# Kernel tuning notes

Measured on AMD Instinct MI355X. Metric: run time of the kernel, lower is better.

## Reference

```python
import jax, jax.numpy as jnp
import numpy as np

NUM_C = 1000
B, L = 8, 1024
D, H, NB, DFF = 512, 8, 4, 2048
DK = D // H
EPS = 1e-5


def _ln(x, s, b):
    mu = jnp.mean(x, axis=-1, keepdims=True)
    var = jnp.mean((x - mu) ** 2, axis=-1, keepdims=True)
    return (x - mu) * jax.lax.rsqrt(var + EPS) * s + b


def setup_inputs() -> dict:
    key = jax.random.key(0)
    ks = iter(jax.random.split(key, 64))

    def nrm(shape, scale=0.02):
        return jax.random.normal(next(ks), shape, dtype=jnp.float32) * scale

    inp = {
        "q": jax.random.randint(next(ks), (B, L), 0, NUM_C),
        "r": jax.random.randint(next(ks), (B, L), 0, 2),
        # embeddings
        "ctx_emb": nrm((NUM_C * 2, D)),
        "val_emb": nrm((NUM_C * 2, D)),
        "skill_emb": nrm((NUM_C, D)),
        "pos_emb": nrm((L, D)),
        # attention projections, stacked over blocks
        "Wq": nrm((NB, D, D)), "bq": jnp.zeros((NB, D)),
        "Wk": nrm((NB, D, D)), "bk": jnp.zeros((NB, D)),
        "Wv": nrm((NB, D, D)), "bv": jnp.zeros((NB, D)),
        "Wo": nrm((NB, D, D)), "bo": jnp.zeros((NB, D)),
        # layer norms (ctx / val streams, pre- and post-FFN)
        "ln1c_s": jnp.ones((NB, D)), "ln1c_b": jnp.zeros((NB, D)),
        "ln1v_s": jnp.ones((NB, D)), "ln1v_b": jnp.zeros((NB, D)),
        "ln2c_s": jnp.ones((NB, D)), "ln2c_b": jnp.zeros((NB, D)),
        "ln2v_s": jnp.ones((NB, D)), "ln2v_b": jnp.zeros((NB, D)),
        # FFNs
        "fc1c_W": nrm((NB, D, DFF)), "fc1c_b": jnp.zeros((NB, DFF)),
        "fc2c_W": nrm((NB, DFF, D)), "fc2c_b": jnp.zeros((NB, D)),
        "fc1v_W": nrm((NB, D, DFF)), "fc1v_b": jnp.zeros((NB, DFF)),
        "fc2v_W": nrm((NB, DFF, D)), "fc2v_b": jnp.zeros((NB, D)),
        # prediction head: [3D -> DFF -> 256 -> 1]
        "hW1": nrm((3 * D, DFF)), "hb1": jnp.zeros((DFF,)),
        "hW2": nrm((DFF, 256)), "hb2": jnp.zeros((256,)),
        "hW3": nrm((256, 1)), "hb3": jnp.zeros((1,)),
    }
    return inp


def reference(q, r, ctx_emb, val_emb, skill_emb, pos_emb,
              Wq, bq, Wk, bk, Wv, bv, Wo, bo,
              ln1c_s, ln1c_b, ln1v_s, ln1v_b,
              ln2c_s, ln2c_b, ln2v_s, ln2v_b,
              fc1c_W, fc1c_b, fc2c_W, fc2c_b,
              fc1v_W, fc1v_b, fc2v_W, fc2v_b,
              hW1, hb1, hW2, hb2, hW3, hb3):
    inter = q + NUM_C * r                       # [B, L] interaction ids
    pos = pos_emb[None, :L, :]
    ctx = ctx_emb[inter] + pos                  # [B, L, D]
    val = val_emb[inter] + pos                  # [B, L, D]
    causal = jnp.tril(jnp.ones((L, L), dtype=bool))
    scale = 1.0 / (DK ** 0.5)

    for i in range(NB):
        # dual-stream MHA: Q,K from ctx; V from val
        Q = (ctx @ Wq[i] + bq[i]).reshape(B, L, H, DK)
        K = (ctx @ Wk[i] + bk[i]).reshape(B, L, H, DK)
        V = (val @ Wv[i] + bv[i]).reshape(B, L, H, DK)
        # fp32 scores (as in torch source), mask==0 -> -inf, softmax
        scores = jnp.einsum('bqhd,bkhd->bhqk', Q.astype(jnp.float32),
                            K.astype(jnp.float32)) * scale
        scores = jnp.where(causal, scores, -jnp.inf)
        attn = jax.nn.softmax(scores, axis=-1)  # dropout = identity (eval)
        out = jnp.einsum('bhqk,bkhd->bqhd', attn, V).reshape(B, L, D)
        out = out @ Wo[i] + bo[i]
        # shared attn output added to both streams, separate norms
        ctx = _ln(ctx + out, ln1c_s[i], ln1c_b[i])
        val = _ln(val + out, ln1v_s[i], ln1v_b[i])
        # dual FFNs
        f_ctx = jax.nn.relu(ctx @ fc1c_W[i] + fc1c_b[i]) @ fc2c_W[i] + fc2c_b[i]
        ctx = _ln(ctx + f_ctx, ln2c_s[i], ln2c_b[i])
        f_val = jax.nn.relu(val @ fc1v_W[i] + fc1v_b[i]) @ fc2v_W[i] + fc2v_b[i]
        val = _ln(val + f_val, ln2v_s[i], ln2v_b[i])

    feat = jnp.concatenate([ctx, val, skill_emb[q]], axis=-1)  # [B, L, 3D]
    h = jax.nn.relu(feat @ hW1 + hb1)
    h = jax.nn.relu(h @ hW2 + hb2)
    logits = (h @ hW3 + hb3)[..., 0]
    return jax.nn.sigmoid(logits)               # [B, L] p(correct)
```

## Files before the change

### kernel.cpp

```cpp
#include <hip/hip_runtime.h>
#include <hip/hip_bf16.h>
#include <math.h>

#define TOK 8192
#define DM 512
#define NH 8
#define DKH 64
#define DFFN 2048
#define SEQ 1024
#define NBLK 4
#define NUMC 1000

typedef __attribute__((ext_vector_type(8))) short bf16x8;
typedef __attribute__((ext_vector_type(4))) float f32x4;
typedef __hip_bfloat16 bf16;

__device__ __forceinline__ void gload_lds16(const ushort* g, ushort* l) {
    __builtin_amdgcn_global_load_lds(
        (const __attribute__((address_space(1))) void*)g,
        (__attribute__((address_space(3))) void*)l, 16, 0, 0);
}

__global__ __launch_bounds__(256) void embed_kernel(
    const int* __restrict__ q, const int* __restrict__ r,
    const float* __restrict__ ctx_emb, const float* __restrict__ val_emb,
    const float* __restrict__ pos_emb,
    float* __restrict__ ctx32, float* __restrict__ val32,
    bf16* __restrict__ ctx16, bf16* __restrict__ val16)
{
    const int t = blockIdx.x;
    const int inter = q[t] + NUMC * r[t];
    const int l = t & (SEQ - 1);
    const float* ce = ctx_emb + (size_t)inter * DM;
    const float* ve = val_emb + (size_t)inter * DM;
    const float* pe = pos_emb + (size_t)l * DM;
    const size_t o = (size_t)t * DM;
    for (int d = threadIdx.x; d < DM; d += 256) {
        float p = pe[d];
        float c = ce[d] + p;
        float v = ve[d] + p;
        ctx32[o + d] = c; val32[o + d] = v;
        ctx16[o + d] = __float2bfloat16(c);
        val16[o + d] = __float2bfloat16(v);
    }
}

__global__ __launch_bounds__(256) void transpose_kernel(
    const float* __restrict__ src, bf16* __restrict__ dst,
    int K, int N, long sb, long db)
{
    __shared__ float t[32][33];
    src += (long)blockIdx.z * sb;
    dst += (long)blockIdx.z * db;
    const int n0 = blockIdx.x * 32;
    const int k0 = blockIdx.y * 32;
    const int tx = threadIdx.x;
    const int ty = threadIdx.y;
    for (int i = ty; i < 32; i += 8) t[i][tx] = src[(size_t)(k0 + i) * N + n0 + tx];
    __syncthreads();
    for (int i = ty; i < 32; i += 8)
        dst[(size_t)(n0 + i) * K + k0 + tx] = __float2bfloat16(t[tx][i]);
}

__global__ __launch_bounds__(256) void vtrans_kernel(
    const bf16* __restrict__ in, bf16* __restrict__ outp)
{
    __shared__ ushort T[64 * 66];
    const int ktile = blockIdx.x;
    const int bh = blockIdx.y;
    const int b = bh >> 3, h = bh & 7;
    const int t = threadIdx.x;
    const int key = t >> 2, c0 = (t & 3) * 16;
    const bf16* src = in + (size_t)(b * SEQ + ktile * 64 + key) * 512 + h * 64 + c0;
    *(bf16x8*)&T[key * 66 + c0] = *(const bf16x8*)src;
    *(bf16x8*)&T[key * 66 + c0 + 8] = *(const bf16x8*)(src + 8);
    __syncthreads();
    const int d = t >> 2, k0 = (t & 3) * 16;
    bf16x8 w0, w1;
#pragma unroll
    for (int j = 0; j < 8; ++j) w0[j] = ((short*)T)[(k0 + j) * 66 + d];
#pragma unroll
    for (int j = 0; j < 8; ++j) w1[j] = ((short*)T)[(k0 + 8 + j) * 66 + d];
    bf16* dst = outp + (size_t)(bh * 64 + d) * SEQ + ktile * 64 + k0;
    *(bf16x8*)dst = w0;
    *(bf16x8*)(dst + 8) = w1;
}

template<int BN, bool OUTBF16>
__global__ __launch_bounds__(256, 2) void mfma_gemm(
    const ushort* __restrict__ A, const ushort* __restrict__ Bt,
    const float* __restrict__ bias1, const float* __restrict__ bias2, int split,
    void* __restrict__ Cv, int N, int K, int relu,
    const ushort* __restrict__ A1, const ushort* __restrict__ Bt1,
    const float* __restrict__ bias1_1, void* __restrict__ Cv1)
{
    if (blockIdx.z) { A = A1; Bt = Bt1; bias1 = bias1_1; Cv = Cv1; }
    constexpr int MI = (BN == 128) ? 4 : 2;
    __shared__ ushort As[128 * 32];
    __shared__ ushort Bs[BN * 32];
    const int tid = threadIdx.x;
    const int wave = tid >> 6;
    const int lane = tid & 63;
    const int ln = lane & 15;
    const int kq = lane >> 4;
    const int nx = gridDim.x;
    const int lin = blockIdx.x + nx * blockIdx.y;
    const int loc = lin >> 3;
    const int mdiv = loc / nx;
    const int bm = ((lin & 7) + 8 * mdiv) * 128;
    const int bn = (loc - mdiv * nx) * BN;
    const int wr = (BN == 128) ? (wave >> 1) * 64 : wave * 32;
    const int wc = (BN == 128) ? (wave & 1) * 64 : 0;

    const int srow = tid >> 2;
    const int scol = (tid & 3) * 8;
    const ushort* Ag0 = A + (size_t)(bm + srow) * K + scol;
    const ushort* Ag1 = A + (size_t)(bm + 64 + srow) * K + scol;
    const ushort* Bg0 = Bt + (size_t)(bn + srow) * K + scol;
    const ushort* Bg1 = (BN == 128) ? (Bt + (size_t)(bn + 64 + srow) * K + scol) : nullptr;
    ushort* AsW0 = As + wave * 512;
    ushort* AsW1 = As + 2048 + wave * 512;
    ushort* BsW0 = Bs + wave * 512;
    ushort* BsW1 = Bs + 2048 + wave * 512;

    f32x4 acc[MI][4];
#pragma unroll
    for (int i = 0; i < MI; ++i)
#pragma unroll
        for (int j = 0; j < 4; ++j) acc[i][j] = (f32x4){0.f, 0.f, 0.f, 0.f};

    for (int k0 = 0; k0 < K; k0 += 32) {
        __syncthreads();
        gload_lds16(Ag0 + k0, AsW0);
        gload_lds16(Ag1 + k0, AsW1);
        gload_lds16(Bg0 + k0, BsW0);
        if (BN == 128) gload_lds16(Bg1 + k0, BsW1);
        __syncthreads();
        bf16x8 bfr[4];
#pragma unroll
        for (int j = 0; j < 4; ++j)
            bfr[j] = *(const bf16x8*)&Bs[(wc + j * 16 + ln) * 32 + kq * 8];
#pragma unroll
        for (int i = 0; i < MI; ++i) {
            const bf16x8 af = *(const bf16x8*)&As[(wr + i * 16 + ln) * 32 + kq * 8];
#pragma unroll
            for (int j = 0; j < 4; ++j)
                acc[i][j] = __builtin_amdgcn_mfma_f32_16x16x32_bf16(af, bfr[j], acc[i][j], 0, 0, 0);
        }
    }

#pragma unroll
    for (int i = 0; i < MI; ++i) {
        const int rowb = bm + wr + i * 16 + kq * 4;
#pragma unroll
        for (int j = 0; j < 4; ++j) {
            const int colg = bn + wc + j * 16 + ln;
            const float bv = (colg < split) ? bias1[colg] : bias2[colg - split];
#pragma unroll
            for (int rr = 0; rr < 4; ++rr) {
                float v = acc[i][j][rr] + bv;
                if (relu) v = fmaxf(v, 0.f);
                if (OUTBF16)
                    ((bf16*)Cv)[(size_t)(rowb + rr) * N + colg] = __float2bfloat16(v);
                else
                    ((float*)Cv)[(size_t)(rowb + rr) * N + colg] = v;
            }
        }
    }
}

__global__ __launch_bounds__(256) void attn_kernel(
    const bf16* __restrict__ QK, const bf16* __restrict__ Vt,
    bf16* __restrict__ Og)
{
    __shared__ ushort Qs[64 * 68];
    __shared__ ushort Ks[64 * 68];
    __shared__ ushort Vs[64 * 68];
    __shared__ ushort Ps[4 * 16 * 68];

    const int tid = threadIdx.x;
    const int wave = tid >> 6, lane = tid & 63;
    const int ln = lane & 15, kq = lane >> 4;
    const int lin = blockIdx.x + 16 * blockIdx.y;
    const int loc = lin >> 3;
    const int qt = loc & 15;
    const int bh = (lin & 7) + 8 * (loc >> 4);
    const int b = bh >> 3, h = bh & 7;

    const int srow = tid >> 2;
    const int sc0 = (tid & 3) * 16;
    {
        const bf16* src = QK + (size_t)(b * SEQ + qt * 64 + srow) * 1024 + h * 64 + sc0;
        *(bf16x8*)&Qs[srow * 68 + sc0] = *(const bf16x8*)src;
        *(bf16x8*)&Qs[srow * 68 + sc0 + 8] = *(const bf16x8*)(src + 8);
    }

    float m2[4], lsum[4];
    f32x4 oacc[4];
#pragma unroll
    for (int r = 0; r < 4; ++r) { m2[r] = -INFINITY; lsum[r] = 0.f; oacc[r] = (f32x4){0.f,0.f,0.f,0.f}; }
    const float sc2 = 0.125f * 1.4426950408889634f;

    for (int kt = 0; kt <= qt; ++kt) {
        __syncthreads();
        {
            const bf16* ksrc = QK + (size_t)(b * SEQ + kt * 64 + srow) * 1024 + 512 + h * 64 + sc0;
            *(bf16x8*)&Ks[srow * 68 + sc0] = *(const bf16x8*)ksrc;
            *(bf16x8*)&Ks[srow * 68 + sc0 + 8] = *(const bf16x8*)(ksrc + 8);
            const bf16* vsrc = Vt + (size_t)(bh * 64 + srow) * SEQ + kt * 64 + sc0;
            *(bf16x8*)&Vs[srow * 68 + sc0] = *(const bf16x8*)vsrc;
            *(bf16x8*)&Vs[srow * 68 + sc0 + 8] = *(const bf16x8*)(vsrc + 8);
        }
        __syncthreads();

        const bf16x8 aq0 = *(const bf16x8*)&Qs[(wave * 16 + ln) * 68 + kq * 8];
        const bf16x8 aq1 = *(const bf16x8*)&Qs[(wave * 16 + ln) * 68 + 32 + kq * 8];
        f32x4 s[4];
#pragma unroll
        for (int c = 0; c < 4; ++c) {
            const bf16x8 bk0 = *(const bf16x8*)&Ks[(c * 16 + ln) * 68 + kq * 8];
            const bf16x8 bk1 = *(const bf16x8*)&Ks[(c * 16 + ln) * 68 + 32 + kq * 8];
            s[c] = (f32x4){0.f, 0.f, 0.f, 0.f};
            s[c] = __builtin_amdgcn_mfma_f32_16x16x32_bf16(aq0, bk0, s[c], 0, 0, 0);
            s[c] = __builtin_amdgcn_mfma_f32_16x16x32_bf16(aq1, bk1, s[c], 0, 0, 0);
        }
        if (kt == qt) {
#pragma unroll
            for (int c = 0; c < 4; ++c)
#pragma unroll
                for (int r = 0; r < 4; ++r) {
                    const int qg = wave * 16 + kq * 4 + r;
                    const int jg = c * 16 + ln;
                    s[c][r] = (jg <= qg) ? s[c][r] * sc2 : -INFINITY;
                }
        } else {
#pragma unroll
            for (int c = 0; c < 4; ++c)
#pragma unroll
                for (int r = 0; r < 4; ++r) s[c][r] *= sc2;
        }
        float alpha[4];
#pragma unroll
        for (int r = 0; r < 4; ++r) {
            float v = fmaxf(fmaxf(s[0][r], s[1][r]), fmaxf(s[2][r], s[3][r]));
            v = fmaxf(v, __shfl_xor(v, 1));
            v = fmaxf(v, __shfl_xor(v, 2));
            v = fmaxf(v, __shfl_xor(v, 4));
            v = fmaxf(v, __shfl_xor(v, 8));
            const float mn = fmaxf(m2[r], v);
            alpha[r] = exp2f(m2[r] - mn);
            m2[r] = mn;
        }
        float rs[4] = {0.f, 0.f, 0.f, 0.f};
#pragma unroll
        for (int c = 0; c < 4; ++c)
#pragma unroll
            for (int r = 0; r < 4; ++r) {
                const float pv = exp2f(s[c][r] - m2[r]);
                rs[r] += pv;
                *(bf16*)&Ps[wave * 1088 + (kq * 4 + r) * 68 + c * 16 + ln] = __float2bfloat16(pv);
            }
#pragma unroll
        for (int r = 0; r < 4; ++r) {
            float v = rs[r];
            v += __shfl_xor(v, 1);
            v += __shfl_xor(v, 2);
            v += __shfl_xor(v, 4);
            v += __shfl_xor(v, 8);
            lsum[r] = lsum[r] * alpha[r] + v;
        }
#pragma unroll
        for (int c2 = 0; c2 < 4; ++c2)
#pragma unroll
            for (int r = 0; r < 4; ++r) oacc[c2][r] *= alpha[r];
        const bf16x8 ap0 = *(const bf16x8*)&Ps[wave * 1088 + ln * 68 + kq * 8];
        const bf16x8 ap1 = *(const bf16x8*)&Ps[wave * 1088 + ln * 68 + 32 + kq * 8];
#pragma unroll
        for (int c2 = 0; c2 < 4; ++c2) {
            const bf16x8 bv0 = *(const bf16x8*)&Vs[(c2 * 16 + ln) * 68 + kq * 8];
            const bf16x8 bv1 = *(const bf16x8*)&Vs[(c2 * 16 + ln) * 68 + 32 + kq * 8];
            oacc[c2] = __builtin_amdgcn_mfma_f32_16x16x32_bf16(ap0, bv0, oacc[c2], 0, 0, 0);
            oacc[c2] = __builtin_amdgcn_mfma_f32_16x16x32_bf16(ap1, bv1, oacc[c2], 0, 0, 0);
        }
    }
    float inv[4];
#pragma unroll
    for (int r = 0; r < 4; ++r) inv[r] = 1.f / lsum[r];
#pragma unroll
    for (int c2 = 0; c2 < 4; ++c2)
#pragma unroll
        for (int r = 0; r < 4; ++r)
            Og[(size_t)(b * SEQ + qt * 64 + wave * 16 + kq * 4 + r) * 512 + h * 64 + c2 * 16 + ln]
                = __float2bfloat16(oacc[c2][r] * inv[r]);
}

__global__ __launch_bounds__(256) void lnp_kernel(
    const float* __restrict__ x0, const bf16* __restrict__ r0, const float* __restrict__ s0,
    const float* __restrict__ b0, float* __restrict__ of0, bf16* __restrict__ oh0,
    const float* __restrict__ x1, const bf16* __restrict__ r1, const float* __restrict__ s1,
    const float* __restrict__ b1, float* __restrict__ of1, bf16* __restrict__ oh1)
{
    const float* x = x0; const bf16* res = r0; const float* s = s0; const float* bb = b0;
    float* of = of0; bf16* oh = oh0;
    if (blockIdx.y) { x = x1; res = r1; s = s1; bb = b1; of = of1; oh = oh1; }
    __shared__ float w1[4], w2[4];
    const size_t o = (size_t)blockIdx.x * DM;
    const int i0 = threadIdx.x, i1 = threadIdx.x + 256;
    const float v0 = x[o + i0] + __bfloat162float(res[o + i0]);
    const float v1 = x[o + i1] + __bfloat162float(res[o + i1]);
    float sum = v0 + v1;
#pragma unroll
    for (int off = 32; off; off >>= 1) sum += __shfl_down(sum, off);
    if ((threadIdx.x & 63) == 0) w1[threadIdx.x >> 6] = sum;
    __syncthreads();
    const float mu = (w1[0] + w1[1] + w1[2] + w1[3]) * (1.f / DM);
    const float d0 = v0 - mu, d1 = v1 - mu;
    float vs = d0 * d0 + d1 * d1;
#pragma unroll
    for (int off = 32; off; off >>= 1) vs += __shfl_down(vs, off);
    if ((threadIdx.x & 63) == 0) w2[threadIdx.x >> 6] = vs;
    __syncthreads();
    const float rstd = rsqrtf((w2[0] + w2[1] + w2[2] + w2[3]) * (1.f / DM) + 1e-5f);
    const float o0 = d0 * rstd * s[i0] + bb[i0];
    const float o1 = d1 * rstd * s[i1] + bb[i1];
    of[o + i0] = o0; of[o + i1] = o1;
    oh[o + i0] = __float2bfloat16(o0);
    oh[o + i1] = __float2bfloat16(o1);
}

__global__ __launch_bounds__(256) void gather_kernel(
    const bf16* __restrict__ ctx16, const bf16* __restrict__ val16,
    const float* __restrict__ skill, const int* __restrict__ q,
    bf16* __restrict__ feat)
{
    const int t = blockIdx.x;
    const float* sp = skill + (size_t)q[t] * DM;
    const bf16* cp = ctx16 + (size_t)t * DM;
    const bf16* vp = val16 + (size_t)t * DM;
    bf16* fp = feat + (size_t)t * (3 * DM);
    for (int d = threadIdx.x; d < DM; d += 256) {
        fp[d] = cp[d];
        fp[DM + d] = vp[d];
        fp[2 * DM + d] = __float2bfloat16(sp[d]);
    }
}

__global__ __launch_bounds__(256) void logits_kernel(
    const float* __restrict__ h2, const float* __restrict__ w,
    const float* __restrict__ bptr, float* __restrict__ out)
{
    __shared__ float w1[4];
    const int t = blockIdx.x;
    float sum = h2[(size_t)t * 256 + threadIdx.x] * w[threadIdx.x];
#pragma unroll
    for (int off = 32; off; off >>= 1) sum += __shfl_down(sum, off);
    if ((threadIdx.x & 63) == 0) w1[threadIdx.x >> 6] = sum;
    __syncthreads();
    if (threadIdx.x == 0) {
        const float logit = w1[0] + w1[1] + w1[2] + w1[3] + bptr[0];
        out[t] = 1.f / (1.f + __expf(-logit));
    }
}

extern "C" void kernel_launch(void* const* d_in, const int* in_sizes, int n_in,
                              void* d_out, int out_size, void* d_ws, size_t ws_size,
                              hipStream_t stream)
{
    const int*   q         = (const int*)d_in[0];
    const int*   r         = (const int*)d_in[1];
    const float* ctx_emb   = (const float*)d_in[2];
    const float* val_emb   = (const float*)d_in[3];
    const float* skill_emb = (const float*)d_in[4];
    const float* pos_emb   = (const float*)d_in[5];
    const float* Wq = (const float*)d_in[6];
    const float* bq = (const float*)d_in[7];
    const float* Wk = (const float*)d_in[8];
    const float* bk = (const float*)d_in[9];
    const float* Wv = (const float*)d_in[10];
    const float* bv = (const float*)d_in[11];
    const float* Wo = (const float*)d_in[12];
    const float* bo = (const float*)d_in[13];
    const float* ln1c_s = (const float*)d_in[14];
    const float* ln1c_b = (const float*)d_in[15];
    const float* ln1v_s = (const float*)d_in[16];
    const float* ln1v_b = (const float*)d_in[17];
    const float* ln2c_s = (const float*)d_in[18];
    const float* ln2c_b = (const float*)d_in[19];
    const float* ln2v_s = (const float*)d_in[20];
    const float* ln2v_b = (const float*)d_in[21];
    const float* fc1c_W = (const float*)d_in[22];
    const float* fc1c_b = (const float*)d_in[23];
    const float* fc2c_W = (const float*)d_in[24];
    const float* fc2c_b = (const float*)d_in[25];
    const float* fc1v_W = (const float*)d_in[26];
    const float* fc1v_b = (const float*)d_in[27];
    const float* fc2v_W = (const float*)d_in[28];
    const float* fc2v_b = (const float*)d_in[29];
    const float* hW1 = (const float*)d_in[30];
    const float* hb1 = (const float*)d_in[31];
    const float* hW2 = (const float*)d_in[32];
    const float* hb2 = (const float*)d_in[33];
    const float* hW3 = (const float*)d_in[34];
    const float* hb3 = (const float*)d_in[35];
    float* out = (float*)d_out;

    char* p = (char*)d_ws;
    auto alloc = [&](size_t bytes) { char* ret = p; p += bytes; return ret; };
    float* ctx32 = (float*)alloc(16777216);
    float* val32 = (float*)alloc(16777216);
    bf16*  ob16c = (bf16*)alloc(8388608);
    bf16*  ob16v = (bf16*)alloc(8388608);
    bf16*  ctx16 = (bf16*)alloc(8388608);
    bf16*  val16 = (bf16*)alloc(8388608);
    bf16*  qk16  = (bf16*)alloc(16777216);
    bf16*  v16   = (bf16*)alloc(8388608);
    bf16*  vt16  = (bf16*)alloc(8388608);
    bf16*  att16 = (bf16*)alloc(8388608);
    bf16*  mid16c = (bf16*)alloc(33554432);
    bf16*  qkT   = (bf16*)alloc(4194304);
    bf16*  vT    = (bf16*)alloc(2097152);
    bf16*  oT    = (bf16*)alloc(2097152);
    bf16*  fc1cT = (bf16*)alloc(8388608);
    bf16*  fc2cT = (bf16*)alloc(8388608);
    bf16*  fc1vT = (bf16*)alloc(8388608);
    bf16*  fc2vT = (bf16*)alloc(8388608);
    bf16*  hW1T  = (bf16*)alloc(6291456);
    bf16*  hW2T  = (bf16*)alloc(1048576);
    bf16*  mid16v = qk16;
    bf16*  feat16 = qk16;
    float* h2     = (float*)vt16;

    const dim3 tb(32, 8);
    transpose_kernel<<<dim3(16, 16, 4), tb, 0, stream>>>(Wq, qkT,          512, 512, 262144, 524288);
    transpose_kernel<<<dim3(16, 16, 4), tb, 0, stream>>>(Wk, qkT + 262144, 512, 512, 262144, 524288);
    transpose_kernel<<<dim3(16, 16, 4), tb, 0, stream>>>(Wv, vT, 512, 512, 262144, 262144);
    transpose_kernel<<<dim3(16, 16, 4), tb, 0, stream>>>(Wo, oT, 512, 512, 262144, 262144);
    transpose_kernel<<<dim3(64, 16, 4), tb, 0, stream>>>(fc1c_W, fc1cT, 512, 2048, 1048576, 1048576);
    transpose_kernel<<<dim3(16, 64, 4), tb, 0, stream>>>(fc2c_W, fc2cT, 2048, 512, 1048576, 1048576);
    transpose_kernel<<<dim3(64, 16, 4), tb, 0, stream>>>(fc1v_W, fc1vT, 512, 2048, 1048576, 1048576);
    transpose_kernel<<<dim3(16, 64, 4), tb, 0, stream>>>(fc2v_W, fc2vT, 2048, 512, 1048576, 1048576);
    transpose_kernel<<<dim3(64, 48, 1), tb, 0, stream>>>(hW1, hW1T, 1536, 2048, 0, 0);
    transpose_kernel<<<dim3(8, 64, 1),  tb, 0, stream>>>(hW2, hW2T, 2048, 256, 0, 0);

    embed_kernel<<<TOK, 256, 0, stream>>>(q, r, ctx_emb, val_emb, pos_emb,
                                          ctx32, val32, ctx16, val16);

    for (int i = 0; i < NBLK; ++i) {
        mfma_gemm<128, true><<<dim3(8, 64), 256, 0, stream>>>(
            (const ushort*)ctx16, (const ushort*)(qkT + (size_t)i * 524288),
            bq + i * DM, bk + i * DM, 512, qk16, 1024, 512, 0,
            nullptr, nullptr, nullptr, nullptr);
        mfma_gemm<64, true><<<dim3(8, 64), 256, 0, stream>>>(
            (const ushort*)val16, (const ushort*)(vT + (size_t)i * 262144),
            bv + i * DM, nullptr, 1 << 30, v16, 512, 512, 0,
            nullptr, nullptr, nullptr, nullptr);
        vtrans_kernel<<<dim3(16, 64), 256, 0, stream>>>(v16, vt16);
        attn_kernel<<<dim3(16, 64), 256, 0, stream>>>(qk16, vt16, att16);
        mfma_gemm<64, true><<<dim3(8, 64), 256, 0, stream>>>(
            (const ushort*)att16, (const ushort*)(oT + (size_t)i * 262144),
            bo + i * DM, nullptr, 1 << 30, ob16c, 512, 512, 0,
            nullptr, nullptr, nullptr, nullptr);
        lnp_kernel<<<dim3(TOK, 2), 256, 0, stream>>>(
            ctx32, ob16c, ln1c_s + i * DM, ln1c_b + i * DM, ctx32, ctx16,
            val32, ob16c, ln1v_s + i * DM, ln1v_b + i * DM, val32, val16);
        mfma_gemm<128, true><<<dim3(16, 64, 2), 256, 0, stream>>>(
            (const ushort*)ctx16, (const ushort*)(fc1cT + (size_t)i * 1048576),
            fc1c_b + i * DFFN, nullptr, 1 << 30, mid16c, 2048, 512, 1,
            (const ushort*)val16, (const ushort*)(fc1vT + (size_t)i * 1048576),
            fc1v_b + i * DFFN, mid16v);
        mfma_gemm<128, true><<<dim3(4, 64, 2), 256, 0, stream>>>(
            (const ushort*)mid16c, (const ushort*)(fc2cT + (size_t)i * 1048576),
            fc2c_b + i * DM, nullptr, 1 << 30, ob16c, 512, 2048, 0,
            (const ushort*)mid16v, (const ushort*)(fc2vT + (size_t)i * 1048576),
            fc2v_b + i * DM, ob16v);
        lnp_kernel<<<dim3(TOK, 2), 256, 0, stream>>>(
            ctx32, ob16c, ln2c_s + i * DM, ln2c_b + i * DM, ctx32, ctx16,
            val32, ob16v, ln2v_s + i * DM, ln2v_b + i * DM, val32, val16);
    }

    gather_kernel<<<TOK, 256, 0, stream>>>(ctx16, val16, skill_emb, q, feat16);
    mfma_gemm<128, true><<<dim3(16, 64), 256, 0, stream>>>(
        (const ushort*)feat16, (const ushort*)hW1T, hb1, nullptr, 1 << 30, mid16c, 2048, 1536, 1,
        nullptr, nullptr, nullptr, nullptr);
    mfma_gemm<64, false><<<dim3(4, 64), 256, 0, stream>>>(
        (const ushort*)mid16c, (const ushort*)hW2T, hb2, nullptr, 1 << 30, h2, 256, 2048, 1,
        nullptr, nullptr, nullptr, nullptr);
    logits_kernel<<<TOK, 256, 0, stream>>>(h2, hW3, hb3, out);
}
```

Before: 1.275 ms.

## Double GEMM K-step with XOR-swizzled LDS and fuse V transpose into GEMM epilogue

```diff
diff --git a/kernel.cpp b/kernel.cpp
--- a/kernel.cpp
+++ b/kernel.cpp
@@ -13,6 +13,7 @@
 
 typedef __attribute__((ext_vector_type(8))) short bf16x8;
 typedef __attribute__((ext_vector_type(4))) float f32x4;
+typedef __attribute__((ext_vector_type(4))) ushort u16x4;
 typedef __hip_bfloat16 bf16;
 
 __device__ __forceinline__ void gload_lds16(const ushort* g, ushort* l) {
@@ -62,42 +63,19 @@
         dst[(size_t)(n0 + i) * K + k0 + tx] = __float2bfloat16(t[tx][i]);
 }
 
-__global__ __launch_bounds__(256) void vtrans_kernel(
-    const bf16* __restrict__ in, bf16* __restrict__ outp)
-{
-    __shared__ ushort T[64 * 66];
-    const int ktile = blockIdx.x;
-    const int bh = blockIdx.y;
-    const int b = bh >> 3, h = bh & 7;
-    const int t = threadIdx.x;
-    const int key = t >> 2, c0 = (t & 3) * 16;
-    const bf16* src = in + (size_t)(b * SEQ + ktile * 64 + key) * 512 + h * 64 + c0;
-    *(bf16x8*)&T[key * 66 + c0] = *(const bf16x8*)src;
-    *(bf16x8*)&T[key * 66 + c0 + 8] = *(const bf16x8*)(src + 8);
-    __syncthreads();
-    const int d = t >> 2, k0 = (t & 3) * 16;
-    bf16x8 w0, w1;
-#pragma unroll
-    for (int j = 0; j < 8; ++j) w0[j] = ((short*)T)[(k0 + j) * 66 + d];
-#pragma unroll
-    for (int j = 0; j < 8; ++j) w1[j] = ((short*)T)[(k0 + 8 + j) * 66 + d];
-    bf16* dst = outp + (size_t)(bh * 64 + d) * SEQ + ktile * 64 + k0;
-    *(bf16x8*)dst = w0;
-    *(bf16x8*)(dst + 8) = w1;
-}
-
 template<int BN, bool OUTBF16>
-__global__ __launch_bounds__(256, 2) void mfma_gemm(
+__global__ __launch_bounds__(256, 3) void mfma_gemm(
     const ushort* __restrict__ A, const ushort* __restrict__ Bt,
     const float* __restrict__ bias1, const float* __restrict__ bias2, int split,
-    void* __restrict__ Cv, int N, int K, int relu,
+    void* __restrict__ Cv, int N, int K, int relu, int vtmode,
     const ushort* __restrict__ A1, const ushort* __restrict__ Bt1,
     const float* __restrict__ bias1_1, void* __restrict__ Cv1)
 {
     if (blockIdx.z) { A = A1; Bt = Bt1; bias1 = bias1_1; Cv = Cv1; }
     constexpr int MI = (BN == 128) ? 4 : 2;
-    __shared__ ushort As[128 * 32];
-    __shared__ ushort Bs[BN * 32];
+    constexpr int BR = BN / 32;
+    __shared__ ushort As[128 * 64];
+    __shared__ ushort Bs[BN * 64];
     const int tid = threadIdx.x;
     const int wave = tid >> 6;
     const int lane = tid & 63;
@@ -112,16 +90,12 @@
     const int wr = (BN == 128) ? (wave >> 1) * 64 : wave * 32;
     const int wc = (BN == 128) ? (wave & 1) * 64 : 0;
 
-    const int srow = tid >> 2;
-    const int scol = (tid & 3) * 8;
-    const ushort* Ag0 = A + (size_t)(bm + srow) * K + scol;
-    const ushort* Ag1 = A + (size_t)(bm + 64 + srow) * K + scol;
-    const ushort* Bg0 = Bt + (size_t)(bn + srow) * K + scol;
-    const ushort* Bg1 = (BN == 128) ? (Bt + (size_t)(bn + 64 + srow) * K + scol) : nullptr;
-    ushort* AsW0 = As + wave * 512;
-    ushort* AsW1 = As + 2048 + wave * 512;
-    ushort* BsW0 = Bs + wave * 512;
-    ushort* BsW1 = Bs + 2048 + wave * 512;
+    const int trow = tid >> 3;
+    const int gcb = (tid & 7) ^ (trow & 7);
+    const ushort* Ab = A + (size_t)(bm + trow) * K + gcb * 8;
+    const ushort* Bb = Bt + (size_t)(bn + trow) * K + gcb * 8;
+    ushort* AsW = As + wave * 512;
+    ushort* BsW = Bs + wave * 512;
 
     f32x4 acc[MI][4];
 #pragma unroll
@@ -129,23 +103,29 @@
 #pragma unroll
         for (int j = 0; j < 4; ++j) acc[i][j] = (f32x4){0.f, 0.f, 0.f, 0.f};
 
-    for (int k0 = 0; k0 < K; k0 += 32) {
+    for (int k0 = 0; k0 < K; k0 += 64) {
         __syncthreads();
-        gload_lds16(Ag0 + k0, AsW0);
-        gload_lds16(Ag1 + k0, AsW1);
-        gload_lds16(Bg0 + k0, BsW0);
-        if (BN == 128) gload_lds16(Bg1 + k0, BsW1);
+#pragma unroll
+        for (int p = 0; p < 4; ++p)
+            gload_lds16(Ab + (size_t)32 * p * K + k0, AsW + p * 2048);
+#pragma unroll
+        for (int p = 0; p < BR; ++p)
+            gload_lds16(Bb + (size_t)32 * p * K + k0, BsW + p * 2048);
         __syncthreads();
-        bf16x8 bfr[4];
-#pragma unroll
-        for (int j = 0; j < 4; ++j)
-            bfr[j] = *(const bf16x8*)&Bs[(wc + j * 16 + ln) * 32 + kq * 8];
-#pragma unroll
-        for (int i = 0; i < MI; ++i) {
-            const bf16x8 af = *(const bf16x8*)&As[(wr + i * 16 + ln) * 32 + kq * 8];
+#pragma unroll
+        for (int half = 0; half < 2; ++half) {
+            const int cb = ((half * 4 + kq) ^ (ln & 7)) * 8;
+            bf16x8 bfr[4];
 #pragma unroll
             for (int j = 0; j < 4; ++j)
-                acc[i][j] = __builtin_amdgcn_mfma_f32_16x16x32_bf16(af, bfr[j], acc[i][j], 0, 0, 0);
+                bfr[j] = *(const bf16x8*)&Bs[(wc + j * 16 + ln) * 64 + cb];
+#pragma unroll
+            for (int i = 0; i < MI; ++i) {
+                const bf16x8 af = *(const bf16x8*)&As[(wr + i * 16 + ln) * 64 + cb];
+#pragma unroll
+                for (int j = 0; j < 4; ++j)
+                    acc[i][j] = __builtin_amdgcn_mfma_f32_16x16x32_bf16(af, bfr[j], acc[i][j], 0, 0, 0);
+            }
         }
     }
 
@@ -156,14 +136,25 @@
         for (int j = 0; j < 4; ++j) {
             const int colg = bn + wc + j * 16 + ln;
             const float bv = (colg < split) ? bias1[colg] : bias2[colg - split];
-#pragma unroll
-            for (int rr = 0; rr < 4; ++rr) {
-                float v = acc[i][j][rr] + bv;
-                if (relu) v = fmaxf(v, 0.f);
-                if (OUTBF16)
-                    ((bf16*)Cv)[(size_t)(rowb + rr) * N + colg] = __float2bfloat16(v);
-                else
-                    ((float*)Cv)[(size_t)(rowb + rr) * N + colg] = v;
+            if (vtmode) {
+                union { u16x4 v; ushort u[4]; } pk;
+#pragma unroll
+                for (int rr = 0; rr < 4; ++rr) {
+                    float v = acc[i][j][rr] + bv;
+                    bf16 t = __float2bfloat16(v);
+                    pk.u[rr] = *(ushort*)&t;
+                }
+                *(u16x4*)((ushort*)Cv + ((size_t)(rowb >> 10) * 512 + colg) * 1024 + (rowb & 1023)) = pk.v;
+            } else {
+#pragma unroll
+                for (int rr = 0; rr < 4; ++rr) {
+                    float v = acc[i][j][rr] + bv;
+                    if (relu) v = fmaxf(v, 0.f);
+                    if (OUTBF16)
+                        ((bf16*)Cv)[(size_t)(rowb + rr) * N + colg] = __float2bfloat16(v);
+                    else
+                        ((float*)Cv)[(size_t)(rowb + rr) * N + colg] = v;
+                }
             }
         }
     }
@@ -413,7 +404,7 @@
     bf16*  ctx16 = (bf16*)alloc(8388608);
     bf16*  val16 = (bf16*)alloc(8388608);
     bf16*  qk16  = (bf16*)alloc(16777216);
-    bf16*  v16   = (bf16*)alloc(8388608);
+    bf16*  v16pad= (bf16*)alloc(8388608);
     bf16*  vt16  = (bf16*)alloc(8388608);
     bf16*  att16 = (bf16*)alloc(8388608);
     bf16*  mid16c = (bf16*)alloc(33554432);
@@ -426,6 +417,7 @@
     bf16*  fc2vT = (bf16*)alloc(8388608);
     bf16*  hW1T  = (bf16*)alloc(6291456);
     bf16*  hW2T  = (bf16*)alloc(1048576);
+    (void)v16pad;
     bf16*  mid16v = qk16;
     bf16*  feat16 = qk16;
     float* h2     = (float*)vt16;
@@ -448,29 +440,28 @@
     for (int i = 0; i < NBLK; ++i) {
         mfma_gemm<128, true><<<dim3(8, 64), 256, 0, stream>>>(
             (const ushort*)ctx16, (const ushort*)(qkT + (size_t)i * 524288),
-            bq + i * DM, bk + i * DM, 512, qk16, 1024, 512, 0,
+            bq + i * DM, bk + i * DM, 512, qk16, 1024, 512, 0, 0,
             nullptr, nullptr, nullptr, nullptr);
         mfma_gemm<64, true><<<dim3(8, 64), 256, 0, stream>>>(
             (const ushort*)val16, (const ushort*)(vT + (size_t)i * 262144),
-            bv + i * DM, nullptr, 1 << 30, v16, 512, 512, 0,
+            bv + i * DM, nullptr, 1 << 30, vt16, 512, 512, 0, 1,
             nullptr, nullptr, nullptr, nullptr);
-        vtrans_kernel<<<dim3(16, 64), 256, 0, stream>>>(v16, vt16);
         attn_kernel<<<dim3(16, 64), 256, 0, stream>>>(qk16, vt16, att16);
         mfma_gemm<64, true><<<dim3(8, 64), 256, 0, stream>>>(
             (const ushort*)att16, (const ushort*)(oT + (size_t)i * 262144),
-            bo + i * DM, nullptr, 1 << 30, ob16c, 512, 512, 0,
+            bo + i * DM, nullptr, 1 << 30, ob16c, 512, 512, 0, 0,
             nullptr, nullptr, nullptr, nullptr);
         lnp_kernel<<<dim3(TOK, 2), 256, 0, stream>>>(
             ctx32, ob16c, ln1c_s + i * DM, ln1c_b + i * DM, ctx32, ctx16,
             val32, ob16c, ln1v_s + i * DM, ln1v_b + i * DM, val32, val16);
         mfma_gemm<128, true><<<dim3(16, 64, 2), 256, 0, stream>>>(
             (const ushort*)ctx16, (const ushort*)(fc1cT + (size_t)i * 1048576),
-            fc1c_b + i * DFFN, nullptr, 1 << 30, mid16c, 2048, 512, 1,
+            fc1c_b + i * DFFN, nullptr, 1 << 30, mid16c, 2048, 512, 1, 0,
             (const ushort*)val16, (const ushort*)(fc1vT + (size_t)i * 1048576),
             fc1v_b + i * DFFN, mid16v);
         mfma_gemm<128, true><<<dim3(4, 64, 2), 256, 0, stream>>>(
             (const ushort*)mid16c, (const ushort*)(fc2cT + (size_t)i * 1048576),
-            fc2c_b + i * DM, nullptr, 1 << 30, ob16c, 512, 2048, 0,
+            fc2c_b + i * DM, nullptr, 1 << 30, ob16c, 512, 2048, 0, 0,
             (const ushort*)mid16v, (const ushort*)(fc2vT + (size_t)i * 1048576),
             fc2v_b + i * DM, ob16v);
         lnp_kernel<<<dim3(TOK, 2), 256, 0, stream>>>(
@@ -480,10 +471,10 @@
 
     gather_kernel<<<TOK, 256, 0, stream>>>(ctx16, val16, skill_emb, q, feat16);
     mfma_gemm<128, true><<<dim3(16, 64), 256, 0, stream>>>(
-        (const ushort*)feat16, (const ushort*)hW1T, hb1, nullptr, 1 << 30, mid16c, 2048, 1536, 1,
+        (const ushort*)feat16, (const ushort*)hW1T, hb1, nullptr, 1 << 30, mid16c, 2048, 1536, 1, 0,
         nullptr, nullptr, nullptr, nullptr);
     mfma_gemm<64, false><<<dim3(4, 64), 256, 0, stream>>>(
-        (const ushort*)mid16c, (const ushort*)hW2T, hb2, nullptr, 1 << 30, h2, 256, 2048, 1,
+        (const ushort*)mid16c, (const ushort*)hW2T, hb2, nullptr, 1 << 30, h2, 256, 2048, 1, 0,
         nullptr, nullptr, nullptr, nullptr);
     logits_kernel<<<TOK, 256, 0, stream>>>(h2, hW3, hb3, out);
 }
```

Result: faster. 1.151 ms (-9.8%).
